# Performance work log

Measured on AMD Instinct MI355X. Metric: run time of the kernel, lower is better.

## Reference

```python
import jax, jax.numpy as jnp
import numpy as np

B, D, H, W = 32, 256, 32, 32
K = 1024

def setup_inputs() -> dict:
    key = jax.random.key(0)
    k1, k2 = jax.random.split(key)
    x = jax.random.normal(k1, (B, D, H, W), dtype=jnp.float32)
    codebook = jax.random.normal(k2, (K, D), dtype=jnp.float32)
    return {"x": x, "codebook": codebook}

def reference(x, codebook):
    b, lat, h, w = x.shape
    # (B, D, H, W) -> (B*H*W, D) tokens
    xt = jnp.transpose(x, (0, 2, 3, 1)).reshape(-1, lat)  # [N, D]
    # Squared euclidean distances via expansion (argmin-equivalent to cdist)
    x_sq = jnp.sum(xt * xt, axis=-1, keepdims=True)           # [N, 1]
    c_sq = jnp.sum(codebook * codebook, axis=-1)[None, :]     # [1, K]
    dist2 = x_sq - 2.0 * (xt @ codebook.T) + c_sq             # [N, K]
    idx = jnp.argmin(dist2, axis=-1)                          # [N]
    quant = codebook[idx]                                     # [N, D]
    codebook_loss = jnp.mean((jax.lax.stop_gradient(xt) - quant) ** 2)
    commitment_loss = jnp.mean((xt - jax.lax.stop_gradient(quant)) ** 2)
    # Straight-through estimator
    out = xt + jax.lax.stop_gradient(quant - xt)              # [N, D]
    out = out.reshape(b, h, w, lat).transpose(0, 3, 1, 2)     # [B, D, H, W]
    min_enc_idx = idx.reshape(b, h, w)                        # [B, H, W]
    return out, min_enc_idx, codebook_loss, commitment_loss
```

## Files before the change

kernel.cpp:

```cpp
#include <hip/hip_runtime.h>

#define B_   32
#define D_   256
#define HW_  1024
#define N_   32768
#define K_   1024
#define DHW  (D_ * HW_)
#define MARGIN 0.3f

typedef __attribute__((ext_vector_type(8)))  short bf16x8;
typedef __attribute__((ext_vector_type(16))) float f32x16;

union FragU { uint4 q; bf16x8 v; };

#define MFMA32 __builtin_amdgcn_mfma_f32_32x32x16_bf16

__device__ inline uint bf16rne(float x) {
    uint ub = __float_as_uint(x);
    return (ub + 0x7fffu + ((ub >> 16) & 1u)) >> 16;
}

__global__ __launch_bounds__(256)
void prep_cb(const float* __restrict__ cb, uint4* __restrict__ cbt2,
             float* __restrict__ csq, float* __restrict__ cbT,
             int* __restrict__ rcount, float* __restrict__ oloss) {
    __shared__ float Lf[16][256];
    const int tid = threadIdx.x;
    const int k0 = blockIdx.x * 16;

    #pragma unroll
    for (int pass = 0; pass < 4; ++pass) {
        int idx = pass * 1024 + tid * 4;
        int r = idx >> 8, d = idx & 255;
        float4 v = *reinterpret_cast<const float4*>(cb + (size_t)(k0 + r) * D_ + d);
        *reinterpret_cast<float4*>(&Lf[r][d]) = v;
    }
    if (blockIdx.x == 0 && tid == 0) { *rcount = 0; oloss[0] = 0.f; oloss[1] = 0.f; }
    __syncthreads();

    {
        const int w = tid >> 6, lane = tid & 63;
        for (int rl = 0; rl < 4; ++rl) {
            int r = w * 4 + rl;
            float parts[4];
            #pragma unroll
            for (int g = 0; g < 4; ++g) {
                float s = Lf[r][g * 64 + lane];
                s = s * s;
                #pragma unroll
                for (int off = 32; off >= 1; off >>= 1) s += __shfl_xor(s, off, 64);
                parts[g] = s;
            }
            if (lane == 0)
                csq[k0 + r] = (parts[0] + parts[1]) + (parts[2] + parts[3]);
        }
    }

    {
        const int chit = tid >> 2, kq = tid & 3;
        const int ch = chit >> 2, it = chit & 3;
        const int p = it >> 1, h = it & 1;
        const int d0 = ch * 16 + h * 8;
        #pragma unroll
        for (int kk = 0; kk < 4; ++kk) {
            int kl = kq * 4 + kk;
            uint wv[4];
            #pragma unroll
            for (int jj = 0; jj < 4; ++jj) {
                float e0 = Lf[kl][d0 + 2 * jj];
                float e1 = Lf[kl][d0 + 2 * jj + 1];
                uint h0 = bf16rne(e0), h1 = bf16rne(e1);
                if (p) {
                    h0 = bf16rne(e0 - __uint_as_float(h0 << 16));
                    h1 = bf16rne(e1 - __uint_as_float(h1 << 16));
                }
                wv[jj] = h0 | (h1 << 16);
            }
            cbt2[((size_t)chit << 10) + k0 + kl] = make_uint4(wv[0], wv[1], wv[2], wv[3]);
        }
    }

    {
        const int d = tid;
        float buf[16];
        #pragma unroll
        for (int kl = 0; kl < 16; ++kl) buf[kl] = Lf[kl][d];
        float* dst = cbT + (size_t)d * K_ + k0;
        #pragma unroll
        for (int q = 0; q < 4; ++q) {
            float4 v4 = make_float4(buf[q * 4], buf[q * 4 + 1], buf[q * 4 + 2], buf[q * 4 + 3]);
            *reinterpret_cast<float4*>(dst + q * 4) = v4;
        }
    }
}

#define DO_STEP(SA, SB, SC, SD, S) do {                                          \
    const int cc_ = cq * 4 + (S);                                                \
    const int ch_ = cc_ & 15;                                                    \
    FragU tf[4];                                                                 \
    _Pragma("unroll")                                                            \
    for (int j = 0; j < 4; ++j) tf[j].q = TkS[ch_ * 2 + sub][j * 32 + l31];      \
    __builtin_amdgcn_s_setprio(1);                                               \
    _Pragma("unroll")                                                            \
    for (int j = 0; j < 4; ++j)                                                  \
        acc[0][j] = MFMA32(SA.v, tf[j].v, acc[0][j], 0, 0, 0);                   \
    _Pragma("unroll")                                                            \
    for (int j = 0; j < 4; ++j)                                                  \
        acc[1][j] = MFMA32(SB.v, tf[j].v, acc[1][j], 0, 0, 0);                   \
    _Pragma("unroll")                                                            \
    for (int j = 0; j < 4; ++j)                                                  \
        acc[0][j] = MFMA32(SC.v, tf[j].v, acc[0][j], 0, 0, 0);                   \
    _Pragma("unroll")                                                            \
    for (int j = 0; j < 4; ++j)                                                  \
        acc[1][j] = MFMA32(SD.v, tf[j].v, acc[1][j], 0, 0, 0);                   \
    __builtin_amdgcn_s_setprio(0);                                               \
    if (cq < 7) {                                                                \
        const int nc_ = cc_ + 4;                                                 \
        const int noff_ = (((nc_ & 15) * 4) << 10) + ((nc_ >> 4) * 64);          \
        SA.q = cb_hi[noff_];      SB.q = cb_hi[noff_ + 32];                      \
        SC.q = cb_lo[noff_];      SD.q = cb_lo[noff_ + 32];                      \
    }                                                                            \
} while (0)

__global__ __launch_bounds__(512, 1)
void vq_main(const float* __restrict__ x, const uint4* __restrict__ cbt2,
             const float* __restrict__ csqg, const float* __restrict__ cb,
             int* __restrict__ rcount, int* __restrict__ rlist,
             float* __restrict__ bdist, float* __restrict__ out,
             float* __restrict__ oidx, float* __restrict__ oloss) {
    __shared__ __align__(16) uint SMEM[17408];
    uint4 (*TkS)[128] = reinterpret_cast<uint4(*)[128]>(SMEM);
    float* csqS = reinterpret_cast<float*>(SMEM + 16384);

    const int tid = threadIdx.x;
    const int lane = tid & 63;
    const int sub = lane >> 5, l31 = lane & 31;
    const int w = tid >> 6;
    const int tok0 = blockIdx.x * 128;
    const int bb = tok0 >> 10, hw0 = tok0 & 1023;

    csqS[tid] = csqg[tid];
    csqS[tid + 512] = csqg[tid + 512];

    const uint4* cb_hi = cbt2 + (sub << 10) + w * 128 + l31;
    const uint4* cb_lo = cbt2 + ((2 + sub) << 10) + w * 128 + l31;

    FragU p0a, p0b, p0c, p0d, p1a, p1b, p1c, p1d,
          p2a, p2b, p2c, p2d, p3a, p3b, p3c, p3d;
    p0a.q = cb_hi[0];         p0b.q = cb_hi[32];
    p0c.q = cb_lo[0];         p0d.q = cb_lo[32];
    p1a.q = cb_hi[1 << 12];   p1b.q = cb_hi[(1 << 12) + 32];
    p1c.q = cb_lo[1 << 12];   p1d.q = cb_lo[(1 << 12) + 32];
    p2a.q = cb_hi[2 << 12];   p2b.q = cb_hi[(2 << 12) + 32];
    p2c.q = cb_lo[2 << 12];   p2d.q = cb_lo[(2 << 12) + 32];
    p3a.q = cb_hi[3 << 12];   p3b.q = cb_hi[(3 << 12) + 32];
    p3c.q = cb_lo[3 << 12];   p3d.q = cb_lo[(3 << 12) + 32];

    {
        const int t = tid & 127;
        const int dgrp = tid >> 7;
        const float* xp = x + (size_t)bb * DHW + hw0 + t;
        #pragma unroll
        for (int i = 0; i < 8; ++i) {
            int g = i * 4 + dgrp;
            float v[8];
            #pragma unroll
            for (int e = 0; e < 8; ++e)
                v[e] = xp[(size_t)(g * 8 + e) * HW_];
            uint wd[4];
            #pragma unroll
            for (int jj = 0; jj < 4; ++jj)
                wd[jj] = bf16rne(v[2 * jj]) | (bf16rne(v[2 * jj + 1]) << 16);
            TkS[g][t] = make_uint4(wd[0], wd[1], wd[2], wd[3]);
        }
    }
    __syncthreads();

    f32x16 acc[2][4] = {};
    float v1[4], v2[4]; int k1[4];
    #pragma unroll
    for (int j = 0; j < 4; ++j) { v1[j] = 3.4e38f; v2[j] = 3.4e38f; k1[j] = 0; }

    for (int cq = 0; cq < 8; ++cq) {
        DO_STEP(p0a, p0b, p0c, p0d, 0);
        DO_STEP(p1a, p1b, p1c, p1d, 1);
        DO_STEP(p2a, p2b, p2c, p2d, 2);
        DO_STEP(p3a, p3b, p3c, p3d, 3);

        if ((cq & 3) == 3) {
            const int ct = cq >> 2;
            const int cbase = w * 128 + ct * 64 + sub * 4;
            #pragma unroll
            for (int f = 0; f < 2; ++f) {
                #pragma unroll
                for (int g8 = 0; g8 < 4; ++g8) {
                    float4 cs4 = *reinterpret_cast<const float4*>(&csqS[cbase + f * 32 + g8 * 8]);
                    const float csa[4] = {cs4.x, cs4.y, cs4.z, cs4.w};
                    #pragma unroll
                    for (int q = 0; q < 4; ++q) {
                        int code = cbase + f * 32 + g8 * 8 + q;
                        int r = g8 * 4 + q;
                        #pragma unroll
                        for (int j = 0; j < 4; ++j) {
                            float s = fmaf(-2.f, acc[f][j][r], csa[q]);
                            bool c = s < v1[j];
                            v2[j] = c ? v1[j] : fminf(v2[j], s);
                            k1[j] = c ? code : k1[j];
                            v1[j] = c ? s : v1[j];
                        }
                    }
                }
            }
            const f32x16 zf = {};
            #pragma unroll
            for (int f = 0; f < 2; ++f)
                #pragma unroll
                for (int j = 0; j < 4; ++j) acc[f][j] = zf;
        }
    }

    #pragma unroll
    for (int j = 0; j < 4; ++j) {
        float ov1 = __shfl_xor(v1[j], 32, 64);
        float ov2 = __shfl_xor(v2[j], 32, 64);
        int   ok1 = __shfl_xor(k1[j], 32, 64);
        float nv2 = fminf(fminf(v2[j], ov2), fmaxf(v1[j], ov1));
        if (ov1 < v1[j] || (ov1 == v1[j] && ok1 < k1[j])) { v1[j] = ov1; k1[j] = ok1; }
        v2[j] = nv2;
    }
    __syncthreads();
    float* red = reinterpret_cast<float*>(SMEM);
    int* bestk_s = reinterpret_cast<int*>(SMEM + 17280);
    if (sub == 0) {
        #pragma unroll
        for (int j = 0; j < 4; ++j) {
            int t = j * 32 + l31;
            red[(w * 128 + t) * 3 + 0] = v1[j];
            red[(w * 128 + t) * 3 + 1] = v2[j];
            red[(w * 128 + t) * 3 + 2] = __int_as_float(k1[j]);
        }
    }
    __syncthreads();
    if (tid < 128) {
        float bv1 = red[tid * 3], bv2 = red[tid * 3 + 1];
        int bk = __float_as_int(red[tid * 3 + 2]);
        #pragma unroll
        for (int m = 1; m < 8; ++m) {
            float a1 = red[(m * 128 + tid) * 3], a2 = red[(m * 128 + tid) * 3 + 1];
            int ak = __float_as_int(red[(m * 128 + tid) * 3 + 2]);
            float nv2 = fminf(fminf(bv2, a2), fmaxf(bv1, a1));
            if (a1 < bv1 || (a1 == bv1 && ak < bk)) { bv1 = a1; bk = ak; }
            bv2 = nv2;
        }
        int n = tok0 + tid;
        bestk_s[tid] = bk;
        bdist[n] = bv1;
        oidx[n] = (float)bk;
        if (bv2 - bv1 < MARGIN) rlist[atomicAdd(rcount, 1)] = n;
        float v = bv1;
        #pragma unroll
        for (int off = 32; off >= 1; off >>= 1) v += __shfl_xor(v, off, 64);
        if ((tid & 63) == 0) {
            float t2 = v * (1.0f / 8388608.0f);
            atomicAdd(&oloss[0], t2);
            atomicAdd(&oloss[1], t2);
        }
    }
    __syncthreads();

    float* S2 = reinterpret_cast<float*>(SMEM);
    #pragma unroll 1
    for (int h = 0; h < 2; ++h) {
        #pragma unroll
        for (int i = 0; i < 8; ++i) {
            int r = w * 8 + i;
            int kk = bestk_s[h * 64 + r];
            float4 cw4 = *reinterpret_cast<const float4*>(cb + (size_t)kk * D_ + lane * 4);
            *reinterpret_cast<float4*>(&S2[r * 260 + lane * 4]) = cw4;
        }
        __syncthreads();
        {
            const int q = tid & 15, dg = tid >> 4;
            const size_t obase = (size_t)bb * DHW + hw0 + h * 64 + q * 4;
            #pragma unroll
            for (int dd = 0; dd < 8; ++dd) {
                int d = dg * 8 + dd;
                float4 wv;
                wv.x = S2[(q * 4 + 0) * 260 + d];
                wv.y = S2[(q * 4 + 1) * 260 + d];
                wv.z = S2[(q * 4 + 2) * 260 + d];
                wv.w = S2[(q * 4 + 3) * 260 + d];
                *reinterpret_cast<float4*>(out + obase + (size_t)d * HW_) = wv;
            }
        }
        __syncthreads();
    }
}

__global__ __launch_bounds__(256)
void vq_refine(const float* __restrict__ x, const float* __restrict__ cb,
               const float* __restrict__ cbT, const float* __restrict__ csq,
               const int* __restrict__ rcount, const int* __restrict__ rlist,
               const float* __restrict__ bdist, float* __restrict__ out,
               float* __restrict__ oidx, float* __restrict__ oloss) {
    __shared__ float xv[8][256];
    __shared__ float xsq[8];
    __shared__ float wredv[4][8];
    __shared__ int   wredk[4][8];
    __shared__ int   kfin[8];
    const int tid = threadIdx.x;
    const int cnt = min(rcount[0], N_);
    for (int base = blockIdx.x * 8; base < cnt; base += gridDim.x * 8) {
        const int m = min(8, cnt - base);
        __syncthreads();
        for (int j = 0; j < m; ++j) {
            int n = rlist[base + j];
            int b = n >> 10, hw = n & 1023;
            xv[j][tid] = x[(size_t)b * DHW + (size_t)tid * HW_ + hw];
        }
        for (int j = m; j < 8; ++j) xv[j][tid] = 0.f;
        __syncthreads();
        {
            int g = tid >> 5, l = tid & 31;
            float s = 0.f;
            #pragma unroll
            for (int d8 = 0; d8 < 8; ++d8) { float v = xv[g][d8 * 32 + l]; s = fmaf(v, v, s); }
            #pragma unroll
            for (int mm = 1; mm < 32; mm <<= 1) s += __shfl_xor(s, mm, 64);
            if (l == 0) xsq[g] = s;
        }
        __syncthreads();

        float dots[4][8];
        #pragma unroll
        for (int c4 = 0; c4 < 4; ++c4)
            #pragma unroll
            for (int j = 0; j < 8; ++j) dots[c4][j] = 0.f;

        const float* cbase = cbT + tid;
        for (int d0 = 0; d0 < 256; d0 += 8) {
            float xr[8][8];
            #pragma unroll
            for (int j = 0; j < 8; ++j) {
                float4 a = *reinterpret_cast<const float4*>(&xv[j][d0]);
                float4 b = *reinterpret_cast<const float4*>(&xv[j][d0 + 4]);
                xr[j][0] = a.x; xr[j][1] = a.y; xr[j][2] = a.z; xr[j][3] = a.w;
                xr[j][4] = b.x; xr[j][5] = b.y; xr[j][6] = b.z; xr[j][7] = b.w;
            }
            #pragma unroll
            for (int c4 = 0; c4 < 4; ++c4) {
                float cv[8];
                #pragma unroll
                for (int u = 0; u < 8; ++u)
                    cv[u] = cbase[(size_t)(d0 + u) * K_ + c4 * 256];
                #pragma unroll
                for (int u = 0; u < 8; ++u)
                    #pragma unroll
                    for (int j = 0; j < 8; ++j)
                        dots[c4][j] = fmaf(cv[u], xr[j][u], dots[c4][j]);
            }
        }

        float bv[8]; int bk[8];
        #pragma unroll
        for (int j = 0; j < 8; ++j) { bv[j] = 3.4e38f; bk[j] = 0; }
        #pragma unroll
        for (int c4 = 0; c4 < 4; ++c4) {
            const int code = c4 * 256 + tid;
            const float cs = csq[code];
            #pragma unroll
            for (int j = 0; j < 8; ++j) {
                float dist = fmaf(-2.f, dots[c4][j], xsq[j]) + cs;
                if (dist < bv[j]) { bv[j] = dist; bk[j] = code; }
            }
        }
        #pragma unroll
        for (int j = 0; j < 8; ++j) {
            if (j < m) {
                float v = bv[j]; int k = bk[j];
                #pragma unroll
                for (int mm = 1; mm < 64; mm <<= 1) {
                    float ov = __shfl_xor(v, mm, 64);
                    int   ok = __shfl_xor(k, mm, 64);
                    if (ov < v || (ov == v && ok < k)) { v = ov; k = ok; }
                }
                if ((tid & 63) == 0) { wredv[tid >> 6][j] = v; wredk[tid >> 6][j] = k; }
            }
        }
        __syncthreads();
        if (tid < m) {
            float v = wredv[0][tid]; int k = wredk[0][tid];
            #pragma unroll
            for (int q = 1; q < 4; ++q) {
                if (wredv[q][tid] < v || (wredv[q][tid] == v && wredk[q][tid] < k)) {
                    v = wredv[q][tid]; k = wredk[q][tid];
                }
            }
            int n = rlist[base + tid];
            kfin[tid] = k;
            oidx[n] = (float)k;
            float delta = (v - bdist[n]) * (1.0f / 8388608.0f);
            atomicAdd(&oloss[0], delta);
            atomicAdd(&oloss[1], delta);
        }
        __syncthreads();
        for (int j = 0; j < m; ++j) {
            int n = rlist[base + j];
            int b = n >> 10, hw = n & 1023;
            out[(size_t)b * DHW + (size_t)tid * HW_ + hw] = cb[(size_t)kfin[j] * D_ + tid];
        }
        __syncthreads();
    }
}

extern "C" void kernel_launch(void* const* d_in, const int* in_sizes, int n_in,
                              void* d_out, int out_size, void* d_ws, size_t ws_size,
                              hipStream_t stream) {
    const float* x  = (const float*)d_in[0];
    const float* cb = (const float*)d_in[1];

    float* out   = (float*)d_out;
    float* oidx  = out + 8388608;
    float* oloss = out + 8388608 + 32768;

    uint* wsb = (uint*)d_ws;
    uint4*  cbt2  = (uint4*)wsb;
    float*  csq   = (float*)(wsb + 262144);
    float*  cbT   = (float*)(wsb + 263168);
    int*    rcount= (int*)  (wsb + 525312);
    int*    rlist = (int*)  (wsb + 525316);
    float*  bdist = (float*)(wsb + 558084);

    prep_cb <<<64, 256, 0, stream>>>(cb, cbt2, csq, cbT, rcount, oloss);
    vq_main <<<256, 512, 0, stream>>>(x, cbt2, csq, cb, rcount, rlist, bdist, out, oidx, oloss);
    vq_refine<<<512, 256, 0, stream>>>(x, cb, cbT, csq, rcount, rlist, bdist, out, oidx, oloss);
}
```

Baseline: 106.3 us.

## Use three-term split-bf16 distances and tighten refinement margin

Splits each token into high and low bf16 parts and adds the codebook-high × token-low MFMA term, so the main distance GEMM is closer to fp32. Because the approximate distances are tighter, the margin that sends ambiguous tokens to the exact fp32 refine pass shrinks, and the refine grid is halved. This trades more MFMA work, a deeper per-step schedule, doubled LDS and a shallower codebook prefetch in the main kernel for fewer tokens needing exact re-evaluation.

```diff
diff --git a/kernel.cpp b/kernel.cpp
--- a/kernel.cpp
+++ b/kernel.cpp
@@ -6,7 +6,7 @@
 #define N_   32768
 #define K_   1024
 #define DHW  (D_ * HW_)
-#define MARGIN 0.3f
+#define MARGIN 0.02f
 
 typedef __attribute__((ext_vector_type(8)))  short bf16x8;
 typedef __attribute__((ext_vector_type(16))) float f32x16;
@@ -94,31 +94,40 @@
     }
 }
 
-#define DO_STEP(SA, SB, SC, SD, S) do {                                          \
-    const int cc_ = cq * 4 + (S);                                                \
-    const int ch_ = cc_ & 15;                                                    \
-    FragU tf[4];                                                                 \
-    _Pragma("unroll")                                                            \
-    for (int j = 0; j < 4; ++j) tf[j].q = TkS[ch_ * 2 + sub][j * 32 + l31];      \
+#define DO_STEP3(DA, DB, DC, DD, S) do {                                         \
+    const int s_ = cq * 2 + (S);                                                 \
+    const int ch_ = s_ & 15;                                                     \
+    FragU tfh[4], tfl[4];                                                        \
+    _Pragma("unroll")                                                            \
+    for (int j = 0; j < 4; ++j) {                                                \
+        tfh[j].q = TkS[ch_ * 2 + sub][j * 32 + l31];                             \
+        tfl[j].q = TkL[ch_ * 2 + sub][j * 32 + l31];                             \
+    }                                                                            \
     __builtin_amdgcn_s_setprio(1);                                               \
     _Pragma("unroll")                                                            \
     for (int j = 0; j < 4; ++j)                                                  \
-        acc[0][j] = MFMA32(SA.v, tf[j].v, acc[0][j], 0, 0, 0);                   \
-    _Pragma("unroll")                                                            \
-    for (int j = 0; j < 4; ++j)                                                  \
-        acc[1][j] = MFMA32(SB.v, tf[j].v, acc[1][j], 0, 0, 0);                   \
-    _Pragma("unroll")                                                            \
-    for (int j = 0; j < 4; ++j)                                                  \
-        acc[0][j] = MFMA32(SC.v, tf[j].v, acc[0][j], 0, 0, 0);                   \
-    _Pragma("unroll")                                                            \
-    for (int j = 0; j < 4; ++j)                                                  \
-        acc[1][j] = MFMA32(SD.v, tf[j].v, acc[1][j], 0, 0, 0);                   \
+        acc[0][j] = MFMA32(DA.v, tfh[j].v, acc[0][j], 0, 0, 0);                  \
+    _Pragma("unroll")                                                            \
+    for (int j = 0; j < 4; ++j)                                                  \
+        acc[1][j] = MFMA32(DB.v, tfh[j].v, acc[1][j], 0, 0, 0);                  \
+    _Pragma("unroll")                                                            \
+    for (int j = 0; j < 4; ++j)                                                  \
+        acc[0][j] = MFMA32(DC.v, tfh[j].v, acc[0][j], 0, 0, 0);                  \
+    _Pragma("unroll")                                                            \
+    for (int j = 0; j < 4; ++j)                                                  \
+        acc[1][j] = MFMA32(DD.v, tfh[j].v, acc[1][j], 0, 0, 0);                  \
+    _Pragma("unroll")                                                            \
+    for (int j = 0; j < 4; ++j)                                                  \
+        acc[0][j] = MFMA32(DA.v, tfl[j].v, acc[0][j], 0, 0, 0);                  \
+    _Pragma("unroll")                                                            \
+    for (int j = 0; j < 4; ++j)                                                  \
+        acc[1][j] = MFMA32(DB.v, tfl[j].v, acc[1][j], 0, 0, 0);                  \
     __builtin_amdgcn_s_setprio(0);                                               \
-    if (cq < 7) {                                                                \
-        const int nc_ = cc_ + 4;                                                 \
+    if (s_ + 2 < 32) {                                                           \
+        const int nc_ = s_ + 2;                                                  \
         const int noff_ = (((nc_ & 15) * 4) << 10) + ((nc_ >> 4) * 64);          \
-        SA.q = cb_hi[noff_];      SB.q = cb_hi[noff_ + 32];                      \
-        SC.q = cb_lo[noff_];      SD.q = cb_lo[noff_ + 32];                      \
+        DA.q = cb_hi[noff_];      DB.q = cb_hi[noff_ + 32];                      \
+        DC.q = cb_lo[noff_];      DD.q = cb_lo[noff_ + 32];                      \
     }                                                                            \
 } while (0)
 
@@ -128,9 +137,10 @@
              int* __restrict__ rcount, int* __restrict__ rlist,
              float* __restrict__ bdist, float* __restrict__ out,
              float* __restrict__ oidx, float* __restrict__ oloss) {
-    __shared__ __align__(16) uint SMEM[17408];
+    __shared__ __align__(16) uint SMEM[33792];
     uint4 (*TkS)[128] = reinterpret_cast<uint4(*)[128]>(SMEM);
-    float* csqS = reinterpret_cast<float*>(SMEM + 16384);
+    uint4 (*TkL)[128] = reinterpret_cast<uint4(*)[128]>(SMEM + 16384);
+    float* csqS = reinterpret_cast<float*>(SMEM + 32768);
 
     const int tid = threadIdx.x;
     const int lane = tid & 63;
@@ -145,16 +155,11 @@
     const uint4* cb_hi = cbt2 + (sub << 10) + w * 128 + l31;
     const uint4* cb_lo = cbt2 + ((2 + sub) << 10) + w * 128 + l31;
 
-    FragU p0a, p0b, p0c, p0d, p1a, p1b, p1c, p1d,
-          p2a, p2b, p2c, p2d, p3a, p3b, p3c, p3d;
-    p0a.q = cb_hi[0];         p0b.q = cb_hi[32];
-    p0c.q = cb_lo[0];         p0d.q = cb_lo[32];
-    p1a.q = cb_hi[1 << 12];   p1b.q = cb_hi[(1 << 12) + 32];
-    p1c.q = cb_lo[1 << 12];   p1d.q = cb_lo[(1 << 12) + 32];
-    p2a.q = cb_hi[2 << 12];   p2b.q = cb_hi[(2 << 12) + 32];
-    p2c.q = cb_lo[2 << 12];   p2d.q = cb_lo[(2 << 12) + 32];
-    p3a.q = cb_hi[3 << 12];   p3b.q = cb_hi[(3 << 12) + 32];
-    p3c.q = cb_lo[3 << 12];   p3d.q = cb_lo[(3 << 12) + 32];
+    FragU d0a, d0b, d0c, d0d, d1a, d1b, d1c, d1d;
+    d0a.q = cb_hi[0];       d0b.q = cb_hi[32];
+    d0c.q = cb_lo[0];       d0d.q = cb_lo[32];
+    d1a.q = cb_hi[4096];    d1b.q = cb_hi[4096 + 32];
+    d1c.q = cb_lo[4096];    d1d.q = cb_lo[4096 + 32];
 
     {
         const int t = tid & 127;
@@ -167,11 +172,18 @@
             #pragma unroll
             for (int e = 0; e < 8; ++e)
                 v[e] = xp[(size_t)(g * 8 + e) * HW_];
-            uint wd[4];
-            #pragma unroll
-            for (int jj = 0; jj < 4; ++jj)
-                wd[jj] = bf16rne(v[2 * jj]) | (bf16rne(v[2 * jj + 1]) << 16);
-            TkS[g][t] = make_uint4(wd[0], wd[1], wd[2], wd[3]);
+            uint wh[4], wl[4];
+            #pragma unroll
+            for (int jj = 0; jj < 4; ++jj) {
+                float e0 = v[2 * jj], e1 = v[2 * jj + 1];
+                uint h0 = bf16rne(e0), h1 = bf16rne(e1);
+                uint l0 = bf16rne(e0 - __uint_as_float(h0 << 16));
+                uint l1 = bf16rne(e1 - __uint_as_float(h1 << 16));
+                wh[jj] = h0 | (h1 << 16);
+                wl[jj] = l0 | (l1 << 16);
+            }
+            TkS[g][t] = make_uint4(wh[0], wh[1], wh[2], wh[3]);
+            TkL[g][t] = make_uint4(wl[0], wl[1], wl[2], wl[3]);
         }
     }
     __syncthreads();
@@ -181,14 +193,12 @@
     #pragma unroll
     for (int j = 0; j < 4; ++j) { v1[j] = 3.4e38f; v2[j] = 3.4e38f; k1[j] = 0; }
 
-    for (int cq = 0; cq < 8; ++cq) {
-        DO_STEP(p0a, p0b, p0c, p0d, 0);
-        DO_STEP(p1a, p1b, p1c, p1d, 1);
-        DO_STEP(p2a, p2b, p2c, p2d, 2);
-        DO_STEP(p3a, p3b, p3c, p3d, 3);
-
-        if ((cq & 3) == 3) {
-            const int ct = cq >> 2;
+    for (int cq = 0; cq < 16; ++cq) {
+        DO_STEP3(d0a, d0b, d0c, d0d, 0);
+        DO_STEP3(d1a, d1b, d1c, d1d, 1);
+
+        if ((cq & 7) == 7) {
+            const int ct = cq >> 3;
             const int cbase = w * 128 + ct * 64 + sub * 4;
             #pragma unroll
             for (int f = 0; f < 2; ++f) {
@@ -230,7 +240,7 @@
     }
     __syncthreads();
     float* red = reinterpret_cast<float*>(SMEM);
-    int* bestk_s = reinterpret_cast<int*>(SMEM + 17280);
+    int* bestk_s = reinterpret_cast<int*>(SMEM + 33600);
     if (sub == 0) {
         #pragma unroll
         for (int j = 0; j < 4; ++j) {
@@ -433,5 +443,5 @@
 
     prep_cb <<<64, 256, 0, stream>>>(cb, cbt2, csq, cbT, rcount, oloss);
     vq_main <<<256, 512, 0, stream>>>(x, cbt2, csq, cb, rcount, rlist, bdist, out, oidx, oloss);
-    vq_refine<<<512, 256, 0, stream>>>(x, cb, cbT, csq, rcount, rlist, bdist, out, oidx, oloss);
+    vq_refine<<<256, 256, 0, stream>>>(x, cb, cbT, csq, rcount, rlist, bdist, out, oidx, oloss);
 }
```

New measurement: 115.3 us. 8.4% more time.
